# Kernel optimization log

Measured on AMD Instinct MI355X. Metric: run time of the kernel, lower is better.

## Reference

```python
import jax, jax.numpy as jnp
import numpy as np

N_USERS = 100000
N_ITEMS = 100000
N_EDGES = 500000
D = 128


def setup_inputs() -> dict:
    key = jax.random.key(0)
    ks = jax.random.split(key, 12)
    def w(k, shape):
        fan_in = shape[0]
        return jax.random.normal(k, shape, dtype=jnp.float32) * (1.0 / np.sqrt(fan_in))
    return {
        "h_user": jax.random.normal(ks[0], (N_USERS, D), dtype=jnp.float32),
        "h_item": jax.random.normal(ks[1], (N_ITEMS, D), dtype=jnp.float32),
        "src": jax.random.randint(ks[2], (N_EDGES,), 0, N_USERS, dtype=jnp.int32),
        "dst": jax.random.randint(ks[3], (N_EDGES,), 0, N_ITEMS, dtype=jnp.int32),
        "W1": w(ks[4], (2 * D, 256)), "b1": jnp.zeros((256,), jnp.float32),
        "W2": w(ks[5], (256, 128)), "b2": jnp.zeros((128,), jnp.float32),
        "W3": w(ks[6], (128, 64)), "b3": jnp.zeros((64,), jnp.float32),
        "W4": w(ks[7], (64, 1)), "b4": jnp.zeros((1,), jnp.float32),
        "Wg1": w(ks[8], (2 * D, 64)), "bg1": jnp.zeros((64,), jnp.float32),
        "Wg2": w(ks[9], (64, 2)), "bg2": jnp.zeros((2,), jnp.float32),
    }


def reference(h_user, h_item, src, dst,
              W1, b1, W2, b2, W3, b3, W4, b4,
              Wg1, bg1, Wg2, bg2):
    # Gather src/dst node embeddings per edge: [E, D] each
    s = h_user[src]
    d = h_item[dst]
    e = jnp.concatenate([s, d], axis=1)  # [E, 2D]

    # Dot-product scores
    dot_scores = jnp.sum(s * d, axis=1)  # [E]

    # MLP scores (3 hidden layers + linear head), dropout in eval mode
    x = jax.nn.relu(e @ W1 + b1)
    x = jax.nn.relu(x @ W2 + b2)
    x = jax.nn.relu(x @ W3 + b3)
    mlp_scores = (x @ W4 + b4)[:, 0]  # [E]

    # Gated fusion: softmax over 2 gates per edge
    g = jax.nn.relu(e @ Wg1 + bg1)
    gates = jax.nn.softmax(g @ Wg2 + bg2, axis=-1)  # [E, 2]
    final = gates[:, 0] * dot_scores + gates[:, 1] * mlp_scores
    return final
```

## Files before the change

### kernel.cpp

```cpp
#include <hip/hip_runtime.h>
#include <hip/hip_bf16.h>
#include <stdint.h>

typedef __bf16 bf16x8 __attribute__((ext_vector_type(8)));
typedef float f32x4 __attribute__((ext_vector_type(4)));
typedef float f32x2 __attribute__((ext_vector_type(2)));
typedef uint32_t u32x4 __attribute__((ext_vector_type(4)));

__device__ __forceinline__ uint32_t swz(uint32_t row, uint32_t col, uint32_t strideB) {
    return (row * strideB + col * 2u) ^ ((row & 7u) << 4);
}
__device__ __forceinline__ unsigned short f2bf_bits(float v) {
    __bf16 h = (__bf16)v; return __builtin_bit_cast(unsigned short, h);
}
__device__ __forceinline__ float bf2f(__bf16 h) { return (float)h; }

#define OFF_BU_E    0
#define OFF_BI_E    40960
#define OFF_W2T_E   81920
#define OFF_W3T_E   114688
#define PREP_TOT    122880
#define OFF_TBL_B   262144

__global__ void prep_weights_fast(const float* __restrict__ W1, const float* __restrict__ Wg1,
                                  const float* __restrict__ W2, const float* __restrict__ W3,
                                  unsigned short* __restrict__ ws) {
    int idx = blockIdx.x * 256 + threadIdx.x;
    if (idx >= PREP_TOT) return;
    float v;
    if (idx < OFF_BI_E) {
        int n = idx >> 7, k = idx & 127;
        v = (n < 256) ? W1[k * 256 + n] : Wg1[k * 64 + (n - 256)];
    } else if (idx < OFF_W2T_E) {
        int loc = idx - OFF_BI_E; int n = loc >> 7, k = loc & 127;
        v = (n < 256) ? W1[(128 + k) * 256 + n] : Wg1[(128 + k) * 64 + (n - 256)];
    } else if (idx < OFF_W3T_E) {
        int loc = idx - OFF_W2T_E; int n = loc >> 8, k = loc & 255;
        v = W2[k * 128 + n];
    } else {
        int loc = idx - OFF_W3T_E; int n = loc >> 7, k = loc & 127;
        v = W3[k * 64 + n];
    }
    ws[idx] = f2bf_bits(v);
}

#define POUT_STRIDE 328
__global__ __launch_bounds__(512, 2)
void proj_kernel(const float* __restrict__ HU, const float* __restrict__ HI,
                 const unsigned short* __restrict__ wsmat,
                 const float* __restrict__ b1, const float* __restrict__ bg1,
                 uint8_t* __restrict__ PU8, uint8_t* __restrict__ PI8,
                 unsigned short* __restrict__ PGU, unsigned short* __restrict__ PGI,
                 unsigned short* __restrict__ HU16, unsigned short* __restrict__ HI16,
                 int nu, int ni, int nbu) {
    __shared__ __align__(16) unsigned short lds[64 * POUT_STRIDE];
    const int t = threadIdx.x, w = t >> 6, l = t & 63, l15 = l & 15, l4 = l >> 4;
    const bool isU = (int)blockIdx.x < nbu;
    const int rb = (isU ? (int)blockIdx.x : (int)blockIdx.x - nbu) * 64;
    const int rows = isU ? nu : ni;
    const float* H = isU ? HU : HI;
    const unsigned short* Bmat = wsmat + (isU ? OFF_BU_E : OFF_BI_E);
    uint8_t* P8 = isU ? PU8 : PI8;
    unsigned short* Pg  = isU ? PGU : PGI;
    unsigned short* H16 = isU ? HU16 : HI16;
    const int addBias = isU ? 1 : 0;

    {
        const int r = t >> 3, q = t & 7;
        int rg = rb + r; int rc = rg < rows ? rg : rows - 1;
        const float* p = H + (size_t)rc * 128 + q * 16;
        f32x4 f0 = *(const f32x4*)(p);     f32x4 f1 = *(const f32x4*)(p + 4);
        f32x4 f2 = *(const f32x4*)(p + 8); f32x4 f3 = *(const f32x4*)(p + 12);
        bf16x8 h0, h1;
        #pragma unroll
        for (int j = 0; j < 4; ++j) {
            h0[j] = (__bf16)f0[j]; h0[j + 4] = (__bf16)f1[j];
            h1[j] = (__bf16)f2[j]; h1[j + 4] = (__bf16)f3[j];
        }
        *(bf16x8*)((char*)lds + swz(r, q * 16, 256)) = h0;
        *(bf16x8*)((char*)lds + swz(r, q * 16 + 8, 256)) = h1;
        if (rg < rows) {
            *(bf16x8*)(H16 + (size_t)rg * 128 + q * 16) = h0;
            *(bf16x8*)(H16 + (size_t)rg * 128 + q * 16 + 8) = h1;
        }
    }
    __syncthreads();
    const int mg = w & 1, cg = w >> 1;
    f32x4 acc[2][5] = {};
    #pragma unroll
    for (int kt = 0; kt < 4; ++kt) {
        bf16x8 aA = *(const bf16x8*)((const char*)lds + swz(mg * 32 + l15, kt * 32 + l4 * 8, 256));
        bf16x8 aB = *(const bf16x8*)((const char*)lds + swz(mg * 32 + 16 + l15, kt * 32 + l4 * 8, 256));
        #pragma unroll
        for (int nt = 0; nt < 5; ++nt) {
            const int n = cg * 80 + nt * 16 + l15;
            bf16x8 bfr = *(const bf16x8*)(Bmat + n * 128 + kt * 32 + l4 * 8);
            acc[0][nt] = __builtin_amdgcn_mfma_f32_16x16x32_bf16(aA, bfr, acc[0][nt], 0, 0, 0);
            acc[1][nt] = __builtin_amdgcn_mfma_f32_16x16x32_bf16(aB, bfr, acc[1][nt], 0, 0, 0);
        }
    }
    __syncthreads();
    #pragma unroll
    for (int nt = 0; nt < 5; ++nt) {
        const int n = cg * 80 + nt * 16 + l15;
        const float bias = addBias ? ((n < 256) ? b1[n] : bg1[n - 256]) : 0.f;
        #pragma unroll
        for (int mt = 0; mt < 2; ++mt) {
            #pragma unroll
            for (int j = 0; j < 4; ++j) {
                const int row = mg * 32 + mt * 16 + l4 * 4 + j;
                lds[row * POUT_STRIDE + n] = f2bf_bits(acc[mt][nt][j] + bias);
            }
        }
    }
    __syncthreads();
    {
        const int r = t >> 3, q = t & 7;
        const int rg = rb + r;
        if (rg < rows) {
            uint32_t dw[8];
            #pragma unroll
            for (int vb = 0; vb < 4; ++vb) {
                bf16x8 pv = *(const bf16x8*)(&lds[r * POUT_STRIDE + q * 32 + vb * 8]);
                float f[8];
                #pragma unroll
                for (int j = 0; j < 8; ++j) f[j] = bf2f(pv[j]);
                uint32_t d0 = 0, d1 = 0;
                d0 = __builtin_amdgcn_cvt_pk_fp8_f32(f[0], f[1], d0, false);
                d0 = __builtin_amdgcn_cvt_pk_fp8_f32(f[2], f[3], d0, true);
                d1 = __builtin_amdgcn_cvt_pk_fp8_f32(f[4], f[5], d1, false);
                d1 = __builtin_amdgcn_cvt_pk_fp8_f32(f[6], f[7], d1, true);
                dw[vb * 2] = d0; dw[vb * 2 + 1] = d1;
            }
            u32x4 s0 = {dw[0], dw[1], dw[2], dw[3]};
            u32x4 s1 = {dw[4], dw[5], dw[6], dw[7]};
            *(u32x4*)(P8 + (size_t)rg * 256 + q * 32)      = s0;
            *(u32x4*)(P8 + (size_t)rg * 256 + q * 32 + 16) = s1;
            bf16x8 gv = *(const bf16x8*)(&lds[r * POUT_STRIDE + 256 + q * 8]);
            *(bf16x8*)(Pg + (size_t)rg * 64 + q * 8) = gv;
        }
    }
}

#define GRID_MAIN 2048

__global__ __launch_bounds__(256, 2)
void edge_main(const int* __restrict__ src, const int* __restrict__ dst,
               const uint8_t* __restrict__ PU8, const uint8_t* __restrict__ PI8,
               const unsigned short* __restrict__ PGU, const unsigned short* __restrict__ PGI,
               const unsigned short* __restrict__ HU16, const unsigned short* __restrict__ HI16,
               const unsigned short* __restrict__ W2T, const unsigned short* __restrict__ W3T,
               const float* __restrict__ b2, const float* __restrict__ b3,
               const float* __restrict__ b4, const float* __restrict__ W4,
               const float* __restrict__ Wg2, const float* __restrict__ bg2,
               float* __restrict__ out, int E) {
    __shared__ __align__(16) unsigned short lds_x1[32 * 256];
    __shared__ __align__(16) unsigned short lds_x2[32 * 128];
    __shared__ float lds_dot[32], lds_g0[32], lds_g1[32];
    __shared__ float lds_mlp[4][32];
    __shared__ float lds_wg0[64], lds_wg1[64];

    const int t = threadIdx.x, w = t >> 6, l = t & 63, l15 = l & 15, l4 = l >> 4;
    const int r = t >> 3, q = t & 7;

    const unsigned short* w2p = W2T + (w * 32 + l15) * 256 + l4 * 8;
    const unsigned short* w3p = W3T + (w * 16 + l15) * 128 + l4 * 8;
    float b2v[2];
    #pragma unroll
    for (int nt = 0; nt < 2; ++nt) b2v[nt] = b2[w * 32 + nt * 16 + l15];
    const float b3v = b3[w * 16 + l15], w4v = W4[w * 16 + l15];
    const float bg2_0 = bg2[0], bg2_1 = bg2[1], b4_0 = b4[0];

    if (t < 64) { lds_wg0[t] = Wg2[t * 2]; lds_wg1[t] = Wg2[t * 2 + 1]; }

    const int NT = (E + 31) >> 5;
    int tile = blockIdx.x;
    if (tile >= NT) return;

    u32x4 gpu8[2], gpi8[2];
    bf16x8 ghu[2], ghi[2], gpg_u, gpg_i;
#define ISSUE(TT) do { \
        int e_ = (TT) * 32 + r; if (e_ >= E) e_ = E - 1; \
        const int sA_ = src[e_], dA_ = dst[e_]; \
        const uint8_t* pu_ = PU8 + (size_t)sA_ * 256 + q * 32; \
        const uint8_t* pi_ = PI8 + (size_t)dA_ * 256 + q * 32; \
        const unsigned short* hu_ = HU16 + (size_t)sA_ * 128 + q * 16; \
        const unsigned short* hi_ = HI16 + (size_t)dA_ * 128 + q * 16; \
        gpu8[0] = *(const u32x4*)(pu_);      gpu8[1] = *(const u32x4*)(pu_ + 16); \
        gpi8[0] = *(const u32x4*)(pi_);      gpi8[1] = *(const u32x4*)(pi_ + 16); \
        ghu[0] = *(const bf16x8*)(hu_);      ghu[1] = *(const bf16x8*)(hu_ + 8); \
        ghi[0] = *(const bf16x8*)(hi_);      ghi[1] = *(const bf16x8*)(hi_ + 8); \
        gpg_u = *(const bf16x8*)(PGU + (size_t)sA_ * 64 + q * 8); \
        gpg_i = *(const bf16x8*)(PGI + (size_t)dA_ * 64 + q * 8); \
    } while (0)

    ISSUE(tile);
    __syncthreads();

    for (;;) {
        #pragma unroll
        for (int v = 0; v < 2; ++v) {
            #pragma unroll
            for (int h = 0; h < 2; ++h) {
                bf16x8 o;
                #pragma unroll
                for (int d = 0; d < 2; ++d) {
                    const uint32_t du = gpu8[v][2 * h + d], di = gpi8[v][2 * h + d];
                    f32x2 a0 = __builtin_amdgcn_cvt_pk_f32_fp8(du, false);
                    f32x2 a1 = __builtin_amdgcn_cvt_pk_f32_fp8(du, true);
                    f32x2 c0 = __builtin_amdgcn_cvt_pk_f32_fp8(di, false);
                    f32x2 c1 = __builtin_amdgcn_cvt_pk_f32_fp8(di, true);
                    o[d * 4 + 0] = (__bf16)fmaxf(a0[0] + c0[0], 0.f);
                    o[d * 4 + 1] = (__bf16)fmaxf(a0[1] + c0[1], 0.f);
                    o[d * 4 + 2] = (__bf16)fmaxf(a1[0] + c1[0], 0.f);
                    o[d * 4 + 3] = (__bf16)fmaxf(a1[1] + c1[1], 0.f);
                }
                *(bf16x8*)((char*)lds_x1 + swz(r, q * 32 + v * 16 + h * 8, 512)) = o;
            }
        }
        {
            float dacc = 0.f;
            #pragma unroll
            for (int v = 0; v < 2; ++v)
                #pragma unroll
                for (int j = 0; j < 8; ++j)
                    dacc += bf2f(ghu[v][j]) * bf2f(ghi[v][j]);
            dacc += __shfl_xor(dacc, 1); dacc += __shfl_xor(dacc, 2); dacc += __shfl_xor(dacc, 4);
            f32x4 wg0a = *(const f32x4*)(&lds_wg0[q * 8]);
            f32x4 wg0b = *(const f32x4*)(&lds_wg0[q * 8 + 4]);
            f32x4 wg1a = *(const f32x4*)(&lds_wg1[q * 8]);
            f32x4 wg1b = *(const f32x4*)(&lds_wg1[q * 8 + 4]);
            float g0 = 0.f, g1 = 0.f;
            #pragma unroll
            for (int i = 0; i < 4; ++i) {
                float va = fmaxf(bf2f(gpg_u[i]) + bf2f(gpg_i[i]), 0.f);
                float vb = fmaxf(bf2f(gpg_u[i + 4]) + bf2f(gpg_i[i + 4]), 0.f);
                g0 += va * wg0a[i] + vb * wg0b[i];
                g1 += va * wg1a[i] + vb * wg1b[i];
            }
            g0 += __shfl_xor(g0, 1); g0 += __shfl_xor(g0, 2); g0 += __shfl_xor(g0, 4);
            g1 += __shfl_xor(g1, 1); g1 += __shfl_xor(g1, 2); g1 += __shfl_xor(g1, 4);
            if (q == 0) { lds_dot[r] = dacc; lds_g0[r] = g0; lds_g1[r] = g1; }
        }
        __syncthreads();

        const int ntile = tile + GRID_MAIN;
        const bool hn = ntile < NT;
        if (hn) ISSUE(ntile);

        {
            f32x4 acc2[2][2] = {};
            #pragma unroll
            for (int kt = 0; kt < 8; ++kt) {
                bf16x8 aA = *(const bf16x8*)((const char*)lds_x1 + swz(l15, kt * 32 + l4 * 8, 512));
                bf16x8 aB = *(const bf16x8*)((const char*)lds_x1 + swz(16 + l15, kt * 32 + l4 * 8, 512));
                bf16x8 bf0 = *(const bf16x8*)(w2p + kt * 32);
                bf16x8 bf1 = *(const bf16x8*)(w2p + 16 * 256 + kt * 32);
                acc2[0][0] = __builtin_amdgcn_mfma_f32_16x16x32_bf16(aA, bf0, acc2[0][0], 0, 0, 0);
                acc2[1][0] = __builtin_amdgcn_mfma_f32_16x16x32_bf16(aB, bf0, acc2[1][0], 0, 0, 0);
                acc2[0][1] = __builtin_amdgcn_mfma_f32_16x16x32_bf16(aA, bf1, acc2[0][1], 0, 0, 0);
                acc2[1][1] = __builtin_amdgcn_mfma_f32_16x16x32_bf16(aB, bf1, acc2[1][1], 0, 0, 0);
            }
            #pragma unroll
            for (int mt = 0; mt < 2; ++mt)
                #pragma unroll
                for (int nt = 0; nt < 2; ++nt) {
                    const int col = w * 32 + nt * 16 + l15;
                    #pragma unroll
                    for (int j = 0; j < 4; ++j) {
                        const int row = mt * 16 + l4 * 4 + j;
                        float v = fmaxf(acc2[mt][nt][j] + b2v[nt], 0.f);
                        *(unsigned short*)((char*)lds_x2 + swz(row, col, 256)) = f2bf_bits(v);
                    }
                }
        }
        __syncthreads();

        {
            f32x4 acc3[2] = {};
            #pragma unroll
            for (int kt = 0; kt < 4; ++kt) {
                bf16x8 a0 = *(const bf16x8*)((const char*)lds_x2 + swz(l15, kt * 32 + l4 * 8, 256));
                bf16x8 a1 = *(const bf16x8*)((const char*)lds_x2 + swz(16 + l15, kt * 32 + l4 * 8, 256));
                bf16x8 bfr = *(const bf16x8*)(w3p + kt * 32);
                acc3[0] = __builtin_amdgcn_mfma_f32_16x16x32_bf16(a0, bfr, acc3[0], 0, 0, 0);
                acc3[1] = __builtin_amdgcn_mfma_f32_16x16x32_bf16(a1, bfr, acc3[1], 0, 0, 0);
            }
            float mp[2][4];
            #pragma unroll
            for (int mt = 0; mt < 2; ++mt)
                #pragma unroll
                for (int j = 0; j < 4; ++j) {
                    mp[mt][j] = fmaxf(acc3[mt][j] + b3v, 0.f) * w4v;
                    mp[mt][j] += __shfl_xor(mp[mt][j], 1);
                    mp[mt][j] += __shfl_xor(mp[mt][j], 2);
                    mp[mt][j] += __shfl_xor(mp[mt][j], 4);
                    mp[mt][j] += __shfl_xor(mp[mt][j], 8);
                }
            if (l15 == 0) {
                #pragma unroll
                for (int mt = 0; mt < 2; ++mt)
                    #pragma unroll
                    for (int j = 0; j < 4; ++j)
                        lds_mlp[w][mt * 16 + l4 * 4 + j] = mp[mt][j];
            }
        }
        __syncthreads();

        if (t < 32) {
            const int e = tile * 32 + t;
            if (e < E) {
                const float mlp = lds_mlp[0][t] + lds_mlp[1][t] + lds_mlp[2][t] + lds_mlp[3][t] + b4_0;
                const float dot = lds_dot[t];
                const float L0 = lds_g0[t] + bg2_0, L1 = lds_g1[t] + bg2_1;
                const float d = L1 - L0;
                const float z = __expf(-fabsf(d));
                const float inv = 1.f / (1.f + z);
                const float g1s = (d >= 0.f) ? inv : z * inv;
                out[e] = (1.f - g1s) * dot + g1s * mlp;
            }
        }
        if (!hn) break;
        __syncthreads();
        tile = ntile;
    }
#undef ISSUE
}

#define FB_ETILE 128
#define FB_WT1_OFF 0
#define FB_WT2_OFF 65536
#define FB_WT3_OFF 98304
#define FB_WTG1_OFF 106496
#define FB_WTOT 122880

__global__ void prep_weights_fb(const float* __restrict__ W1, const float* __restrict__ W2,
                                const float* __restrict__ W3, const float* __restrict__ Wg1,
                                unsigned short* __restrict__ ws) {
    int idx = blockIdx.x * 256 + threadIdx.x;
    if (idx >= FB_WTOT) return;
    float v;
    if (idx < FB_WT2_OFF)      { int n = idx >> 8, k = idx & 255; v = W1[k * 256 + n]; }
    else if (idx < FB_WT3_OFF) { int loc = idx - FB_WT2_OFF; int n = loc >> 8, k = loc & 255; v = W2[k * 128 + n]; }
    else if (idx < FB_WTG1_OFF){ int loc = idx - FB_WT3_OFF; int n = loc >> 7, k = loc & 127; v = W3[k * 64 + n]; }
    else                       { int loc = idx - FB_WTG1_OFF; int n = loc >> 8, k = loc & 255; v = Wg1[k * 64 + n]; }
    ws[idx] = f2bf_bits(v);
}

__global__ __launch_bounds__(512, 2)
void fused_edge_kernel_fb(const float* __restrict__ h_user, const float* __restrict__ h_item,
                          const int* __restrict__ src, const int* __restrict__ dst,
                          const unsigned short* __restrict__ wsmat,
                          const float* __restrict__ b1, const float* __restrict__ b2,
                          const float* __restrict__ b3, const float* __restrict__ b4,
                          const float* __restrict__ W4, const float* __restrict__ bg1,
                          const float* __restrict__ Wg2, const float* __restrict__ bg2,
                          float* __restrict__ out, int E) {
    __shared__ __align__(16) unsigned short lds_e[FB_ETILE * 256];
    __shared__ __align__(16) unsigned short lds_x1[FB_ETILE * 256];
    __shared__ float lds_dot[FB_ETILE];
    const unsigned short* wt1  = wsmat + FB_WT1_OFF;
    const unsigned short* wt2  = wsmat + FB_WT2_OFF;
    const unsigned short* wt3  = wsmat + FB_WT3_OFF;
    const unsigned short* wtg1 = wsmat + FB_WTG1_OFF;
    const int t = threadIdx.x, eb = blockIdx.x * FB_ETILE;
    const int w = t >> 6, l = t & 63, l15 = l & 15, l4 = l >> 4;
    {
        const int r = t >> 2, q = t & 3;
        int e = eb + r; if (e >= E) e = E - 1;
        const int idx = (q < 2) ? src[e] : dst[e];
        const float* rowp = ((q < 2) ? h_user : h_item) + (size_t)idx * 128 + (q & 1) * 64;
        const uint32_t cbase = (uint32_t)q * 64u;
        #pragma unroll
        for (int i = 0; i < 8; ++i) {
            f32x4 a = *reinterpret_cast<const f32x4*>(rowp + i * 8);
            f32x4 b = *reinterpret_cast<const f32x4*>(rowp + i * 8 + 4);
            bf16x8 p;
            #pragma unroll
            for (int j = 0; j < 4; ++j) { p[j] = (__bf16)a[j]; p[j + 4] = (__bf16)b[j]; }
            *reinterpret_cast<bf16x8*>((char*)lds_e + swz(r, cbase + i * 8u, 512)) = p;
        }
    }
    __syncthreads();
    {
        const int r = t >> 2, q = t & 3;
        float acc = 0.f;
        #pragma unroll
        for (int i = 0; i < 4; ++i) {
            uint32_t c = (uint32_t)q * 32u + i * 8u;
            bf16x8 sv = *reinterpret_cast<const bf16x8*>((const char*)lds_e + swz(r, c, 512));
            bf16x8 dv = *reinterpret_cast<const bf16x8*>((const char*)lds_e + swz(r, 128u + c, 512));
            #pragma unroll
            for (int j = 0; j < 8; ++j) acc += (float)sv[j] * (float)dv[j];
        }
        acc += __shfl_xor(acc, 1); acc += __shfl_xor(acc, 2);
        if (q == 0) lds_dot[r] = acc;
    }
    {
        const int mg = w >> 2, cg = w & 3;
        f32x4 acc[4][4] = {};
        #pragma unroll
        for (int kh = 0; kh < 2; ++kh) {
            bf16x8 afr[4][4];
            #pragma unroll
            for (int mt = 0; mt < 4; ++mt)
                #pragma unroll
                for (int kt = 0; kt < 4; ++kt)
                    afr[mt][kt] = *reinterpret_cast<const bf16x8*>((const char*)lds_e +
                        swz(mg * 64 + mt * 16 + l15, kh * 128 + kt * 32 + l4 * 8, 512));
            #pragma unroll
            for (int nt = 0; nt < 4; ++nt) {
                const int n = cg * 64 + nt * 16 + l15;
                #pragma unroll
                for (int kt = 0; kt < 4; ++kt) {
                    bf16x8 bfr = *reinterpret_cast<const bf16x8*>(wt1 + n * 256 + kh * 128 + kt * 32 + l4 * 8);
                    #pragma unroll
                    for (int mt = 0; mt < 4; ++mt)
                        acc[mt][nt] = __builtin_amdgcn_mfma_f32_16x16x32_bf16(afr[mt][kt], bfr, acc[mt][nt], 0, 0, 0);
                }
            }
        }
        #pragma unroll
        for (int nt = 0; nt < 4; ++nt) {
            const int col = cg * 64 + nt * 16 + l15;
            const float bias = b1[col];
            #pragma unroll
            for (int mt = 0; mt < 4; ++mt) {
                const int row0 = mg * 64 + mt * 16 + l4 * 4;
                #pragma unroll
                for (int j = 0; j < 4; ++j) {
                    float v = fmaxf(acc[mt][nt][j] + bias, 0.f);
                    *reinterpret_cast<unsigned short*>((char*)lds_x1 + swz(row0 + j, col, 512)) = f2bf_bits(v);
                }
            }
        }
    }
    float l0p[4] = {0, 0, 0, 0}, l1p[4] = {0, 0, 0, 0};
    {
        bf16x8 ag[8];
        #pragma unroll
        for (int kt = 0; kt < 8; ++kt)
            ag[kt] = *reinterpret_cast<const bf16x8*>((const char*)lds_e + swz(w * 16 + l15, kt * 32 + l4 * 8, 512));
        f32x4 accg[4] = {};
        #pragma unroll
        for (int nt = 0; nt < 4; ++nt) {
            const int n = nt * 16 + l15;
            #pragma unroll
            for (int kt = 0; kt < 8; ++kt) {
                bf16x8 bfr = *reinterpret_cast<const bf16x8*>(wtg1 + n * 256 + kt * 32 + l4 * 8);
                accg[nt] = __builtin_amdgcn_mfma_f32_16x16x32_bf16(ag[kt], bfr, accg[nt], 0, 0, 0);
            }
        }
        #pragma unroll
        for (int nt = 0; nt < 4; ++nt) {
            const int col = nt * 16 + l15;
            const float bg = bg1[col];
            const float w0 = Wg2[col * 2 + 0], w1 = Wg2[col * 2 + 1];
            #pragma unroll
            for (int j = 0; j < 4; ++j) {
                float v = fmaxf(accg[nt][j] + bg, 0.f);
                l0p[j] += v * w0; l1p[j] += v * w1;
            }
        }
        #pragma unroll
        for (int j = 0; j < 4; ++j)
            #pragma unroll
            for (int m = 1; m < 16; m <<= 1) {
                l0p[j] += __shfl_xor(l0p[j], m);
                l1p[j] += __shfl_xor(l1p[j], m);
            }
    }
    __syncthreads();
    {
        const int mg = w >> 1, cg = w & 1;
        bf16x8 a2[2][8];
        #pragma unroll
        for (int mt = 0; mt < 2; ++mt)
            #pragma unroll
            for (int kt = 0; kt < 8; ++kt)
                a2[mt][kt] = *reinterpret_cast<const bf16x8*>((const char*)lds_x1 +
                    swz(mg * 32 + mt * 16 + l15, kt * 32 + l4 * 8, 512));
        f32x4 acc2[2][4] = {};
        #pragma unroll
        for (int nt = 0; nt < 4; ++nt) {
            const int n = cg * 64 + nt * 16 + l15;
            #pragma unroll
            for (int kt = 0; kt < 8; ++kt) {
                bf16x8 bfr = *reinterpret_cast<const bf16x8*>(wt2 + n * 256 + kt * 32 + l4 * 8);
                #pragma unroll
                for (int mt = 0; mt < 2; ++mt)
                    acc2[mt][nt] = __builtin_amdgcn_mfma_f32_16x16x32_bf16(a2[mt][kt], bfr, acc2[mt][nt], 0, 0, 0);
            }
        }
        #pragma unroll
        for (int nt = 0; nt < 4; ++nt) {
            const int col = cg * 64 + nt * 16 + l15;
            const float bias = b2[col];
            #pragma unroll
            for (int mt = 0; mt < 2; ++mt) {
                const int row0 = mg * 32 + mt * 16 + l4 * 4;
                #pragma unroll
                for (int j = 0; j < 4; ++j) {
                    float v = fmaxf(acc2[mt][nt][j] + bias, 0.f);
                    *reinterpret_cast<unsigned short*>((char*)lds_e + swz(row0 + j, col, 256)) = f2bf_bits(v);
                }
            }
        }
    }
    __syncthreads();
    {
        float mlpp[4] = {0, 0, 0, 0};
        bf16x8 a3[4];
        #pragma unroll
        for (int kt = 0; kt < 4; ++kt)
            a3[kt] = *reinterpret_cast<const bf16x8*>((const char*)lds_e + swz(w * 16 + l15, kt * 32 + l4 * 8, 256));
        f32x4 acc3[4] = {};
        #pragma unroll
        for (int nt = 0; nt < 4; ++nt) {
            const int n = nt * 16 + l15;
            #pragma unroll
            for (int kt = 0; kt < 4; ++kt) {
                bf16x8 bfr = *reinterpret_cast<const bf16x8*>(wt3 + n * 128 + kt * 32 + l4 * 8);
                acc3[nt] = __builtin_amdgcn_mfma_f32_16x16x32_bf16(a3[kt], bfr, acc3[nt], 0, 0, 0);
            }
        }
        #pragma unroll
        for (int nt = 0; nt < 4; ++nt) {
            const int col = nt * 16 + l15;
            const float b3v = b3[col];
            const float w4v = W4[col];
            #pragma unroll
            for (int j = 0; j < 4; ++j) {
                float v = fmaxf(acc3[nt][j] + b3v, 0.f);
                mlpp[j] += v * w4v;
            }
        }
        #pragma unroll
        for (int j = 0; j < 4; ++j)
            #pragma unroll
            for (int m = 1; m < 16; m <<= 1)
                mlpp[j] += __shfl_xor(mlpp[j], m);
        if (l15 == 0) {
            #pragma unroll
            for (int j = 0; j < 4; ++j) {
                const int rr = w * 16 + l4 * 4 + j;
                const int e = eb + rr;
                if (e < E) {
                    const float dot = lds_dot[rr];
                    const float mlp = mlpp[j] + b4[0];
                    const float L0 = l0p[j] + bg2[0];
                    const float L1 = l1p[j] + bg2[1];
                    const float d = L1 - L0;
                    const float z = __expf(-fabsf(d));
                    const float inv = 1.f / (1.f + z);
                    const float g1 = (d >= 0.f) ? inv : z * inv;
                    out[e] = (1.f - g1) * dot + g1 * mlp;
                }
            }
        }
    }
}

extern "C" void kernel_launch(void* const* d_in, const int* in_sizes, int n_in,
                              void* d_out, int out_size, void* d_ws, size_t ws_size,
                              hipStream_t stream) {
    const float* h_user = (const float*)d_in[0];
    const float* h_item = (const float*)d_in[1];
    const int*   src    = (const int*)d_in[2];
    const int*   dst    = (const int*)d_in[3];
    const float* W1  = (const float*)d_in[4];
    const float* b1  = (const float*)d_in[5];
    const float* W2  = (const float*)d_in[6];
    const float* b2  = (const float*)d_in[7];
    const float* W3  = (const float*)d_in[8];
    const float* b3  = (const float*)d_in[9];
    const float* W4  = (const float*)d_in[10];
    const float* b4  = (const float*)d_in[11];
    const float* Wg1 = (const float*)d_in[12];
    const float* bg1 = (const float*)d_in[13];
    const float* Wg2 = (const float*)d_in[14];
    const float* bg2 = (const float*)d_in[15];
    const int E  = in_sizes[2];
    const int nu = in_sizes[0] / 128;
    const int ni = in_sizes[1] / 128;

    unsigned short* ws = (unsigned short*)d_ws;
    char* wsb = (char*)d_ws;

    size_t off = OFF_TBL_B;
    uint8_t* PU8 = (uint8_t*)(wsb + off); off += (size_t)nu * 256;
    uint8_t* PI8 = (uint8_t*)(wsb + off); off += (size_t)ni * 256;
    unsigned short* PGU  = (unsigned short*)(wsb + off); off += (size_t)nu * 128;
    unsigned short* PGI  = (unsigned short*)(wsb + off); off += (size_t)ni * 128;
    unsigned short* HU16 = (unsigned short*)(wsb + off); off += (size_t)nu * 256;
    unsigned short* HI16 = (unsigned short*)(wsb + off); off += (size_t)ni * 256;
    const size_t need_bytes = off;

    if (ws_size >= need_bytes) {
        prep_weights_fast<<<(PREP_TOT + 255) / 256, 256, 0, stream>>>(W1, Wg1, W2, W3, ws);
        const int nbu = (nu + 63) / 64, nbi = (ni + 63) / 64;
        proj_kernel<<<nbu + nbi, 512, 0, stream>>>(h_user, h_item, ws, b1, bg1,
                                                   PU8, PI8, PGU, PGI, HU16, HI16, nu, ni, nbu);
        edge_main<<<GRID_MAIN, 256, 0, stream>>>(src, dst, PU8, PI8, PGU, PGI, HU16, HI16,
                                                 ws + OFF_W2T_E, ws + OFF_W3T_E,
                                                 b2, b3, b4, W4, Wg2, bg2, (float*)d_out, E);
    } else {
        prep_weights_fb<<<(FB_WTOT + 255) / 256, 256, 0, stream>>>(W1, W2, W3, Wg1, ws);
        const int nblk = (E + FB_ETILE - 1) / FB_ETILE;
        fused_edge_kernel_fb<<<nblk, 512, 0, stream>>>(h_user, h_item, src, dst, ws,
                                                       b1, b2, b3, b4, W4, bg1, Wg2, bg2,
                                                       (float*)d_out, E);
    }
}
```

Before: 216.6 us.

## Double-buffer per-edge scratch and replace syncthreads with LDS-only barriers

Switches the small per-tile scratch arrays (dot, gate logits, MLP partials) to double buffers indexed by a parity bit, which allows removing the trailing barrier at the end of each tile iteration. The remaining barriers become a custom barrier that waits only on LDS counters and not on outstanding global loads, so the prefetch of the next tile's gathers can stay in flight across the barriers. The prefetch issue also moves before the first barrier. The risk is ordering hazards: lds_x1 is rewritten on the next iteration without a trailing barrier, and correctness depends on the following barriers plus the compiler's waitcnt placement.

```diff
diff --git a/kernel.cpp b/kernel.cpp
--- a/kernel.cpp
+++ b/kernel.cpp
@@ -14,6 +14,13 @@
     __bf16 h = (__bf16)v; return __builtin_bit_cast(unsigned short, h);
 }
 __device__ __forceinline__ float bf2f(__bf16 h) { return (float)h; }
+
+__device__ __forceinline__ void barrier_noflush() {
+    asm volatile("s_waitcnt lgkmcnt(0)" ::: "memory");
+    __builtin_amdgcn_s_barrier();
+    asm volatile("" ::: "memory");
+    __builtin_amdgcn_sched_barrier(0);
+}
 
 #define OFF_BU_E    0
 #define OFF_BI_E    40960
@@ -156,8 +163,8 @@
                float* __restrict__ out, int E) {
     __shared__ __align__(16) unsigned short lds_x1[32 * 256];
     __shared__ __align__(16) unsigned short lds_x2[32 * 128];
-    __shared__ float lds_dot[32], lds_g0[32], lds_g1[32];
-    __shared__ float lds_mlp[4][32];
+    __shared__ float lds_dot[2][32], lds_g0[2][32], lds_g1[2][32];
+    __shared__ float lds_mlp[2][4][32];
     __shared__ float lds_wg0[64], lds_wg1[64];
 
     const int t = threadIdx.x, w = t >> 6, l = t & 63, l15 = l & 15, l4 = l >> 4;
@@ -197,6 +204,7 @@
     ISSUE(tile);
     __syncthreads();
 
+    int pb = 0;
     for (;;) {
         #pragma unroll
         for (int v = 0; v < 2; ++v) {
@@ -240,13 +248,13 @@
             }
             g0 += __shfl_xor(g0, 1); g0 += __shfl_xor(g0, 2); g0 += __shfl_xor(g0, 4);
             g1 += __shfl_xor(g1, 1); g1 += __shfl_xor(g1, 2); g1 += __shfl_xor(g1, 4);
-            if (q == 0) { lds_dot[r] = dacc; lds_g0[r] = g0; lds_g1[r] = g1; }
-        }
-        __syncthreads();
-
+            if (q == 0) { lds_dot[pb][r] = dacc; lds_g0[pb][r] = g0; lds_g1[pb][r] = g1; }
+        }
         const int ntile = tile + GRID_MAIN;
         const bool hn = ntile < NT;
         if (hn) ISSUE(ntile);
+
+        barrier_noflush();
 
         {
             f32x4 acc2[2][2] = {};
@@ -274,7 +282,7 @@
                     }
                 }
         }
-        __syncthreads();
+        barrier_noflush();
 
         {
             f32x4 acc3[2] = {};
@@ -302,17 +310,18 @@
                 for (int mt = 0; mt < 2; ++mt)
                     #pragma unroll
                     for (int j = 0; j < 4; ++j)
-                        lds_mlp[w][mt * 16 + l4 * 4 + j] = mp[mt][j];
-            }
-        }
-        __syncthreads();
+                        lds_mlp[pb][w][mt * 16 + l4 * 4 + j] = mp[mt][j];
+            }
+        }
+        barrier_noflush();
 
         if (t < 32) {
             const int e = tile * 32 + t;
             if (e < E) {
-                const float mlp = lds_mlp[0][t] + lds_mlp[1][t] + lds_mlp[2][t] + lds_mlp[3][t] + b4_0;
-                const float dot = lds_dot[t];
-                const float L0 = lds_g0[t] + bg2_0, L1 = lds_g1[t] + bg2_1;
+                const float mlp = lds_mlp[pb][0][t] + lds_mlp[pb][1][t] + lds_mlp[pb][2][t]
+                                + lds_mlp[pb][3][t] + b4_0;
+                const float dot = lds_dot[pb][t];
+                const float L0 = lds_g0[pb][t] + bg2_0, L1 = lds_g1[pb][t] + bg2_1;
                 const float d = L1 - L0;
                 const float z = __expf(-fabsf(d));
                 const float inv = 1.f / (1.f + z);
@@ -321,8 +330,8 @@
             }
         }
         if (!hn) break;
-        __syncthreads();
         tile = ntile;
+        pb ^= 1;
     }
 #undef ISSUE
 }
```

After: 323.0 us. 1.49x slower.

## Fuse layer-3 and final gating into two waves, drop two barriers per tile

Applied to the files above, without the earlier changes.

Layer 3 is now computed by only two waves, each owning 16 full rows and all 64 output columns. Each wave finishes the W4 reduction and the gated output write itself, so the cross-wave lds_mlp reduction and its barrier go away. The dot and gate scratch arrays are double-buffered with a ping-pong index, which lets the barrier at the end of each loop iteration be removed. The cost is that half the waves sit idle during layer 3, and the safety of the ordering between the layer-1 LDS writes and the layer-3 reads now rests on the remaining barriers.

```diff
diff --git a/kernel.cpp b/kernel.cpp
--- a/kernel.cpp
+++ b/kernel.cpp
@@ -156,19 +156,19 @@
                float* __restrict__ out, int E) {
     __shared__ __align__(16) unsigned short lds_x1[32 * 256];
     __shared__ __align__(16) unsigned short lds_x2[32 * 128];
-    __shared__ float lds_dot[32], lds_g0[32], lds_g1[32];
-    __shared__ float lds_mlp[4][32];
+    __shared__ float lds_dot[2][32], lds_g0[2][32], lds_g1[2][32];
     __shared__ float lds_wg0[64], lds_wg1[64];
 
     const int t = threadIdx.x, w = t >> 6, l = t & 63, l15 = l & 15, l4 = l >> 4;
     const int r = t >> 3, q = t & 7;
 
     const unsigned short* w2p = W2T + (w * 32 + l15) * 256 + l4 * 8;
-    const unsigned short* w3p = W3T + (w * 16 + l15) * 128 + l4 * 8;
     float b2v[2];
     #pragma unroll
     for (int nt = 0; nt < 2; ++nt) b2v[nt] = b2[w * 32 + nt * 16 + l15];
-    const float b3v = b3[w * 16 + l15], w4v = W4[w * 16 + l15];
+    float b3v4[4], w4v4[4];
+    #pragma unroll
+    for (int nt = 0; nt < 4; ++nt) { b3v4[nt] = b3[nt * 16 + l15]; w4v4[nt] = W4[nt * 16 + l15]; }
     const float bg2_0 = bg2[0], bg2_1 = bg2[1], b4_0 = b4[0];
 
     if (t < 64) { lds_wg0[t] = Wg2[t * 2]; lds_wg1[t] = Wg2[t * 2 + 1]; }
@@ -197,6 +197,7 @@
     ISSUE(tile);
     __syncthreads();
 
+    int pb = 0;
     for (;;) {
         #pragma unroll
         for (int v = 0; v < 2; ++v) {
@@ -240,7 +241,7 @@
             }
             g0 += __shfl_xor(g0, 1); g0 += __shfl_xor(g0, 2); g0 += __shfl_xor(g0, 4);
             g1 += __shfl_xor(g1, 1); g1 += __shfl_xor(g1, 2); g1 += __shfl_xor(g1, 4);
-            if (q == 0) { lds_dot[r] = dacc; lds_g0[r] = g0; lds_g1[r] = g1; }
+            if (q == 0) { lds_dot[pb][r] = dacc; lds_g0[pb][r] = g0; lds_g1[pb][r] = g1; }
         }
         __syncthreads();
 
@@ -276,53 +277,51 @@
         }
         __syncthreads();
 
-        {
-            f32x4 acc3[2] = {};
+        if (w < 2) {
+            f32x4 acc3[4] = {};
             #pragma unroll
             for (int kt = 0; kt < 4; ++kt) {
-                bf16x8 a0 = *(const bf16x8*)((const char*)lds_x2 + swz(l15, kt * 32 + l4 * 8, 256));
-                bf16x8 a1 = *(const bf16x8*)((const char*)lds_x2 + swz(16 + l15, kt * 32 + l4 * 8, 256));
-                bf16x8 bfr = *(const bf16x8*)(w3p + kt * 32);
-                acc3[0] = __builtin_amdgcn_mfma_f32_16x16x32_bf16(a0, bfr, acc3[0], 0, 0, 0);
-                acc3[1] = __builtin_amdgcn_mfma_f32_16x16x32_bf16(a1, bfr, acc3[1], 0, 0, 0);
-            }
-            float mp[2][4];
-            #pragma unroll
-            for (int mt = 0; mt < 2; ++mt)
+                bf16x8 a0 = *(const bf16x8*)((const char*)lds_x2 + swz(w * 16 + l15, kt * 32 + l4 * 8, 256));
+                #pragma unroll
+                for (int nt = 0; nt < 4; ++nt) {
+                    bf16x8 bfr = *(const bf16x8*)(W3T + (nt * 16 + l15) * 128 + kt * 32 + l4 * 8);
+                    acc3[nt] = __builtin_amdgcn_mfma_f32_16x16x32_bf16(a0, bfr, acc3[nt], 0, 0, 0);
+                }
+            }
+            float mp[4];
+            #pragma unroll
+            for (int j = 0; j < 4; ++j) {
+                float s = 0.f;
+                #pragma unroll
+                for (int nt = 0; nt < 4; ++nt)
+                    s += fmaxf(acc3[nt][j] + b3v4[nt], 0.f) * w4v4[nt];
+                s += __shfl_xor(s, 1);
+                s += __shfl_xor(s, 2);
+                s += __shfl_xor(s, 4);
+                s += __shfl_xor(s, 8);
+                mp[j] = s;
+            }
+            if (l15 == 0) {
                 #pragma unroll
                 for (int j = 0; j < 4; ++j) {
-                    mp[mt][j] = fmaxf(acc3[mt][j] + b3v, 0.f) * w4v;
-                    mp[mt][j] += __shfl_xor(mp[mt][j], 1);
-                    mp[mt][j] += __shfl_xor(mp[mt][j], 2);
-                    mp[mt][j] += __shfl_xor(mp[mt][j], 4);
-                    mp[mt][j] += __shfl_xor(mp[mt][j], 8);
-                }
-            if (l15 == 0) {
-                #pragma unroll
-                for (int mt = 0; mt < 2; ++mt)
-                    #pragma unroll
-                    for (int j = 0; j < 4; ++j)
-                        lds_mlp[w][mt * 16 + l4 * 4 + j] = mp[mt][j];
-            }
-        }
-        __syncthreads();
-
-        if (t < 32) {
-            const int e = tile * 32 + t;
-            if (e < E) {
-                const float mlp = lds_mlp[0][t] + lds_mlp[1][t] + lds_mlp[2][t] + lds_mlp[3][t] + b4_0;
-                const float dot = lds_dot[t];
-                const float L0 = lds_g0[t] + bg2_0, L1 = lds_g1[t] + bg2_1;
-                const float d = L1 - L0;
-                const float z = __expf(-fabsf(d));
-                const float inv = 1.f / (1.f + z);
-                const float g1s = (d >= 0.f) ? inv : z * inv;
-                out[e] = (1.f - g1s) * dot + g1s * mlp;
+                    const int row = w * 16 + l4 * 4 + j;
+                    const int e = tile * 32 + row;
+                    if (e < E) {
+                        const float mlp = mp[j] + b4_0;
+                        const float dot = lds_dot[pb][row];
+                        const float L0 = lds_g0[pb][row] + bg2_0, L1 = lds_g1[pb][row] + bg2_1;
+                        const float d = L1 - L0;
+                        const float z = __expf(-fabsf(d));
+                        const float inv = 1.f / (1.f + z);
+                        const float g1s = (d >= 0.f) ? inv : z * inv;
+                        out[e] = (1.f - g1s) * dot + g1s * mlp;
+                    }
+                }
             }
         }
         if (!hn) break;
-        __syncthreads();
         tile = ntile;
+        pb ^= 1;
     }
 #undef ISSUE
 }
```

Measured after the change: 257.7 us. 19.0% more time.
